# Performance work log

Hardware: AMD Instinct MI355X
Metric: run time of the kernel (lower is better)

## Reference

```python
import jax, jax.numpy as jnp
import numpy as np

BLANK = 59  # CFG['pad_phrase'] == blank_index == label pad value
NEG = jnp.float32(-1e30)  # -inf surrogate safe for logaddexp


def setup_inputs() -> dict:
    key = jax.random.key(0)
    k1, k2 = jax.random.split(key)
    B, T, V, L = 1024, 384, 60, 45
    labels = jax.random.randint(k1, (B, L), 0, BLANK, dtype=jnp.int32)
    logits = jax.random.normal(k2, (B, T, V), dtype=jnp.float32)
    return {"labels": labels, "logits": logits}


def _ctc_loss(logits, labels):
    # logits: [B, T, V] (not time-major), labels: [B, L] padded with BLANK
    B, T, V = logits.shape
    L = labels.shape[1]
    S = 2 * L + 1  # extended label length: blanks interleaved

    logp = jax.nn.log_softmax(logits, axis=-1)  # tf.nn.ctc_loss softmaxes internally

    # extended label sequence: [blank, l1, blank, l2, ..., blank]
    ext = jnp.full((B, S), BLANK, dtype=jnp.int32).at[:, 1::2].set(labels)
    # per-step emission log-probs for each extended-label position: [B, T, S]
    emit = jnp.take_along_axis(logp, ext[:, None, :], axis=2)

    # skip transition s-2 -> s allowed iff s >= 2, ext[s] != blank, ext[s] != ext[s-2]
    ext_m2 = jnp.pad(ext[:, :-2], ((0, 0), (2, 0)), constant_values=-1)
    skip_ok = (jnp.arange(S) >= 2) & (ext != BLANK) & (ext != ext_m2)

    # alpha init at t=0: only positions 0 (blank) and 1 (first label) reachable
    alpha0 = jnp.full((B, S), NEG).at[:, 0].set(emit[:, 0, 0]).at[:, 1].set(emit[:, 0, 1])

    def step(alpha, emit_t):
        s1 = jnp.pad(alpha[:, :-1], ((0, 0), (1, 0)), constant_values=NEG)
        s2 = jnp.where(skip_ok, jnp.pad(alpha[:, :-2], ((0, 0), (2, 0)), constant_values=NEG), NEG)
        alpha = jnp.logaddexp(jnp.logaddexp(alpha, s1), s2) + emit_t
        return alpha, None

    emit_tbs = jnp.swapaxes(emit, 0, 1)  # [T, B, S]
    alpha_T, _ = jax.lax.scan(step, alpha0, emit_tbs[1:])

    # label_length = number of non-pad tokens (as in the TF layer)
    label_len = jnp.sum((labels != BLANK).astype(jnp.int32), axis=-1)
    end = 2 * label_len  # index of final blank in extended sequence
    a_blank = jnp.take_along_axis(alpha_T, end[:, None], axis=1)[:, 0]
    a_label = jnp.take_along_axis(alpha_T, jnp.maximum(end - 1, 0)[:, None], axis=1)[:, 0]
    a_label = jnp.where(end > 0, a_label, NEG)
    nll = -jnp.logaddexp(a_blank, a_label)  # [B]
    return jnp.mean(nll)


def reference(labels, logits):
    return _ctc_loss(logits, labels)
```

## Files before the change

kernel.cpp:

```cpp
#include <hip/hip_runtime.h>
#include <hip/hip_fp16.h>

#define BLANKC 59

typedef _Float16 half8 __attribute__((ext_vector_type(8)));

__device__ __forceinline__ float wave_shr1(float x, float fill) {
    int r = __builtin_amdgcn_update_dpp(__float_as_int(fill), __float_as_int(x),
                                        0x138 , 0xF, 0xF, false);
    return __int_as_float(r);
}

template <int CTRL>
__device__ __forceinline__ float dpp_fmax(float x) {
    int r = __builtin_amdgcn_update_dpp(__float_as_int(x), __float_as_int(x),
                                        CTRL, 0xF, 0xF, false);
    return fmaxf(x, __int_as_float(r));
}

__device__ __forceinline__ float wave_max_bcast(float x) {
    x = dpp_fmax<0x111>(x);
    x = dpp_fmax<0x112>(x);
    x = dpp_fmax<0x114>(x);
    x = dpp_fmax<0x118>(x);
    x = dpp_fmax<0x142>(x);
    x = dpp_fmax<0x143>(x);
    return __int_as_float(__builtin_amdgcn_readlane(__float_as_int(x), 63));
}

#define TTILE 64
__global__ __launch_bounds__(256)
void ctc_emit(const int* __restrict__ labels, const float* __restrict__ logits,
              __half* __restrict__ em, int T, int V, int L) {
    const int tiles_per_b = 384 / TTILE;
    const int b  = blockIdx.x / tiles_per_b;
    const int t0 = (blockIdx.x % tiles_per_b) * TTILE;
    const int tid = threadIdx.x;

    __shared__ float ftile[TTILE][61];
    __shared__ __half otile[48][72];

    const float* src = logits + ((long)b * T + t0) * V;
    #pragma unroll
    for (int it = 0; it < 15; ++it) {
        const int idx = it * 256 + tid;
        const int r = idx / 60, c = idx - r * 60;
        ftile[r][c] = src[idx];
    }
    __syncthreads();

    {
        const int t = tid >> 2;
        const int q = tid & 3;
        float s = 0.f;
        #pragma unroll
        for (int k = 0; k < 15; ++k) s += __expf(ftile[t][q * 15 + k]);
        s += __shfl_xor(s, 1, 64);
        s += __shfl_xor(s, 2, 64);
        const float lse = __logf(s);
        const int* lab = labels + (long)b * L;
        #pragma unroll
        for (int j = 0; j < 12; ++j) {
            const int l = q * 12 + j;
            if (l < 46) {
                const int v = (l < 45) ? lab[l] : BLANKC;
                otile[l][t] = __float2half(__expf(ftile[t][v] - lse));
            }
        }
    }
    __syncthreads();

    for (int i = tid; i < 46 * 8; i += 256) {
        const int slot = i >> 3, seg = i & 7;
        const float4 v = *(const float4*)&otile[slot][seg * 8];
        float4* dst = (float4*)(em + ((long)b * 48 + slot) * T + t0 + seg * 8);
        *dst = v;
    }
}

#define RS 400
__global__ __launch_bounds__(64)
void ctc_alpha(const int* __restrict__ labels, const __half* __restrict__ em,
               float* __restrict__ out, int T, int L, float inv_b) {
    const int b    = blockIdx.x;
    const int lane = threadIdx.x;

    __shared__ __half S[47 * RS];

    const __half* emb = em + (long)b * 48 * T;
    const int NSEG = T / 8;
    for (int i = lane; i < 46 * NSEG; i += 64) {
        const int r = i / NSEG, seg = i - r * NSEG;
        const half8 v = *(const half8*)(emb + r * T + seg * 8);
        *(half8*)(&S[r * RS + seg * 8]) = v;
    }
    for (int i = lane; i < T; i += 64) S[46 * RS + i] = __float2half(0.f);
    __syncthreads();

    const int* lab = labels + (long)b * L;
    const int labL = (lane < L) ? lab[lane] : BLANKC;
    const int labP = (lane >= 1 && lane < L) ? lab[lane - 1] : BLANKC;
    const float skipf = ((lane >= 1) && (lane < L) && (labL != BLANKC) && (labL != labP))
                        ? 1.0f : 0.0f;

    unsigned long long mk = __ballot((lane < L) && (labL != BLANKC));
    const int len = __popcll(mk);

    const __half* zrow = &S[46 * RS];
    const __half* rowL = (lane < 45) ? &S[lane * RS] : zrow;
    const __half* rowB = (lane < 46) ? &S[45 * RS] : zrow;

    half8 curL = *(const half8*)(rowL);
    half8 curB = *(const half8*)(rowB);

    float a0 = (lane == 0) ? (float)curB[0] * 0x1p80f : 0.f;
    float a1 = (lane == 0) ? (float)curL[0] * 0x1p80f : 0.f;
    int esum = 80;

    auto step = [&](float eL, float eB) {
        const float p   = wave_shr1(a1, 0.0f);
        const float t1  = a0 + a1;
        const float na0 = (a0 + p) * eB;
        const float na1 = fmaf(skipf, p, t1) * eL;
        a0 = na0; a1 = na1;
    };

    auto renorm = [&]() {
        const float m = wave_max_bcast(fmaxf(a0, a1));
        const int e = (__float_as_int(m) >> 23) & 0xff;
        int sexp = 207 - e;
        if (sexp > 127) sexp = 127;
        const float sc = __int_as_float((sexp + 127) << 23);
        a0 *= sc; a1 *= sc;
        esum += sexp;
    };

    half8 nL = *(const half8*)(rowL + 8);
    half8 nB = *(const half8*)(rowB + 8);
    #pragma unroll
    for (int i = 1; i < 8; ++i) step((float)curL[i], (float)curB[i]);
    renorm();

    for (int c = 1; c < NSEG - 1; ++c) {
        const half8 cL = nL, cB = nB;
        nL = *(const half8*)(rowL + (c + 1) * 8);
        nB = *(const half8*)(rowB + (c + 1) * 8);
        #pragma unroll
        for (int i = 0; i < 8; ++i) step((float)cL[i], (float)cB[i]);
        renorm();
    }
    #pragma unroll
    for (int i = 0; i < 8; ++i) step((float)nL[i], (float)nB[i]);

    const float ab2 = __shfl(a0, len, 64);
    float al2 = __shfl(a1, (len > 0) ? len - 1 : 0, 64);
    al2 = (len > 0) ? al2 : 0.f;
    if (lane == 0) {
        const float s   = ab2 + al2;
        const float nll = -(__logf(s) - (float)esum * 0.69314718056f);
        atomicAdd(out, nll * inv_b);
    }
}

extern "C" void kernel_launch(void* const* d_in, const int* in_sizes, int n_in,
                              void* d_out, int out_size, void* d_ws, size_t ws_size,
                              hipStream_t stream) {
    const int* labels   = (const int*)d_in[0];
    const float* logits = (const float*)d_in[1];
    float* out          = (float*)d_out;
    __half* em          = (__half*)d_ws;

    const int L = 45, V = 60;
    const int B = in_sizes[0] / L;
    const int T = in_sizes[1] / (B * V);

    hipMemsetAsync(out, 0, (size_t)out_size * sizeof(float), stream);
    ctc_emit<<<B * (T / TTILE), 256, 0, stream>>>(labels, logits, em, T, V, L);
    ctc_alpha<<<B, 64, 0, stream>>>(labels, em, out, T, L, 1.0f / (float)B);
}
```

Before: 182.2 us.

## Fuse emission softmax and CTC alpha recursion into one kernel via shared memory

Merges the emission kernel and the alpha-recursion kernel into one block per batch item. The 256-thread block loops over time tiles, computes log-softmax emissions, and writes them straight into the shared-memory table the alpha scan reads, so the fp16 workspace round-trip through global memory and the second launch go away. The trade-off is that three of four waves sit idle during the serial alpha scan. Each block also uses more LDS (ftile plus S), which may reduce occupancy and serialise emission loads within each batch item.

Measured after the change: 170.9 us. -6.2%, faster.

```diff
diff --git a/kernel.cpp b/kernel.cpp
--- a/kernel.cpp
+++ b/kernel.cpp
@@ -29,77 +29,59 @@
 }
 
 #define TTILE 64
+#define RS 392
+
 __global__ __launch_bounds__(256)
-void ctc_emit(const int* __restrict__ labels, const float* __restrict__ logits,
-              __half* __restrict__ em, int T, int V, int L) {
-    const int tiles_per_b = 384 / TTILE;
-    const int b  = blockIdx.x / tiles_per_b;
-    const int t0 = (blockIdx.x % tiles_per_b) * TTILE;
+void ctc_fused(const int* __restrict__ labels, const float* __restrict__ logits,
+               float* __restrict__ out, int T, int V, int L, float inv_b) {
+    const int b   = blockIdx.x;
     const int tid = threadIdx.x;
 
-    __shared__ float ftile[TTILE][61];
-    __shared__ __half otile[48][72];
+    __shared__ float  ftile[TTILE][61];
+    __shared__ __half S[47 * RS];
+    __shared__ int    labs[64];
 
-    const float* src = logits + ((long)b * T + t0) * V;
-    #pragma unroll
-    for (int it = 0; it < 15; ++it) {
-        const int idx = it * 256 + tid;
-        const int r = idx / 60, c = idx - r * 60;
-        ftile[r][c] = src[idx];
-    }
-    __syncthreads();
+    if (tid < 64) labs[tid] = (tid < L) ? labels[(long)b * L + tid] : BLANKC;
+    for (int i = tid; i < T; i += 256) S[46 * RS + i] = __float2half(0.f);
 
-    {
-        const int t = tid >> 2;
-        const int q = tid & 3;
-        float s = 0.f;
+    const float* src = logits + (long)b * T * V;
+    const int ntile = T / TTILE;
+    for (int tile = 0; tile < ntile; ++tile) {
+        const float* s0 = src + (long)tile * TTILE * V;
         #pragma unroll
-        for (int k = 0; k < 15; ++k) s += __expf(ftile[t][q * 15 + k]);
-        s += __shfl_xor(s, 1, 64);
-        s += __shfl_xor(s, 2, 64);
-        const float lse = __logf(s);
-        const int* lab = labels + (long)b * L;
-        #pragma unroll
-        for (int j = 0; j < 12; ++j) {
-            const int l = q * 12 + j;
-            if (l < 46) {
-                const int v = (l < 45) ? lab[l] : BLANKC;
-                otile[l][t] = __float2half(__expf(ftile[t][v] - lse));
+        for (int it = 0; it < 15; ++it) {
+            const int idx = it * 256 + tid;
+            const int r = idx / 60, c = idx - r * 60;
+            ftile[r][c] = s0[idx];
+        }
+        __syncthreads();
+        {
+            const int t = tid >> 2;
+            const int q = tid & 3;
+            float s = 0.f;
+            #pragma unroll
+            for (int k = 0; k < 15; ++k) s += __expf(ftile[t][q * 15 + k]);
+            s += __shfl_xor(s, 1, 64);
+            s += __shfl_xor(s, 2, 64);
+            const float lse = __logf(s);
+            const int tg = tile * TTILE + t;
+            #pragma unroll
+            for (int j = 0; j < 12; ++j) {
+                const int l = q * 12 + j;
+                if (l < 46) {
+                    const int v = (l < 45) ? labs[l] : BLANKC;
+                    S[l * RS + tg] = __float2half(__expf(ftile[t][v] - lse));
+                }
             }
         }
+        __syncthreads();
     }
-    __syncthreads();
 
-    for (int i = tid; i < 46 * 8; i += 256) {
-        const int slot = i >> 3, seg = i & 7;
-        const float4 v = *(const float4*)&otile[slot][seg * 8];
-        float4* dst = (float4*)(em + ((long)b * 48 + slot) * T + t0 + seg * 8);
-        *dst = v;
-    }
-}
+    if (tid >= 64) return;
+    const int lane = tid;
 
-#define RS 400
-__global__ __launch_bounds__(64)
-void ctc_alpha(const int* __restrict__ labels, const __half* __restrict__ em,
-               float* __restrict__ out, int T, int L, float inv_b) {
-    const int b    = blockIdx.x;
-    const int lane = threadIdx.x;
-
-    __shared__ __half S[47 * RS];
-
-    const __half* emb = em + (long)b * 48 * T;
-    const int NSEG = T / 8;
-    for (int i = lane; i < 46 * NSEG; i += 64) {
-        const int r = i / NSEG, seg = i - r * NSEG;
-        const half8 v = *(const half8*)(emb + r * T + seg * 8);
-        *(half8*)(&S[r * RS + seg * 8]) = v;
-    }
-    for (int i = lane; i < T; i += 64) S[46 * RS + i] = __float2half(0.f);
-    __syncthreads();
-
-    const int* lab = labels + (long)b * L;
-    const int labL = (lane < L) ? lab[lane] : BLANKC;
-    const int labP = (lane >= 1 && lane < L) ? lab[lane - 1] : BLANKC;
+    const int labL = (lane < L) ? labs[lane] : BLANKC;
+    const int labP = (lane >= 1 && lane < L) ? labs[lane - 1] : BLANKC;
     const float skipf = ((lane >= 1) && (lane < L) && (labL != BLANKC) && (labL != labP))
                         ? 1.0f : 0.0f;
 
@@ -135,6 +117,8 @@
         esum += sexp;
     };
 
+    const int NSEG = T / 8;
+
     half8 nL = *(const half8*)(rowL + 8);
     half8 nB = *(const half8*)(rowB + 8);
     #pragma unroll
@@ -168,13 +152,12 @@
     const int* labels   = (const int*)d_in[0];
     const float* logits = (const float*)d_in[1];
     float* out          = (float*)d_out;
-    __half* em          = (__half*)d_ws;
+    (void)d_ws; (void)ws_size;
 
     const int L = 45, V = 60;
     const int B = in_sizes[0] / L;
     const int T = in_sizes[1] / (B * V);
 
     hipMemsetAsync(out, 0, (size_t)out_size * sizeof(float), stream);
-    ctc_emit<<<B * (T / TTILE), 256, 0, stream>>>(labels, logits, em, T, V, L);
-    ctc_alpha<<<B, 64, 0, stream>>>(labels, em, out, T, L, 1.0f / (float)B);
+    ctc_fused<<<B, 256, 0, stream>>>(labels, logits, out, T, V, L, 1.0f / (float)B);
 }
```
